# Kernel optimization log

Hardware: AMD Instinct MI355X
Metric: run time of the kernel (lower is better)

The kernel has to match this reference:

```python
import jax, jax.numpy as jnp
import numpy as np


def setup_inputs() -> dict:
    key = jax.random.key(0)
    k1, k2 = jax.random.split(key)
    B, S, D, K = 16, 2048, 256, 512
    features = jax.random.normal(k1, (B, S, D), dtype=jnp.float32)
    Ck = jax.random.normal(k2, (1, K, D), dtype=jnp.float32)
    return {"features": features, "Ck": Ck}


def reference(features, Ck):
    # features: (B, S, D); Ck: (1, K, D)
    # Squared euclidean distance to each of K centers: (B, S, K)
    # Computed as ||f||^2 + ||c||^2 - 2 f.c to avoid the (B*S, K, D) diff tensor.
    C = Ck[0]                                   # (K, D)
    f_sq = jnp.sum(features * features, axis=-1, keepdims=True)   # (B, S, 1)
    c_sq = jnp.sum(C * C, axis=-1)                                # (K,)
    cross = jnp.einsum("bsd,kd->bsk", features, C)               # (B, S, K)
    return f_sq + c_sq[None, None, :] - 2.0 * cross
```

## Files before the change

### kernel.cpp

```cpp
#include <hip/hip_runtime.h>

typedef __attribute__((ext_vector_type(8))) short bf16x8;
typedef __attribute__((ext_vector_type(4))) float f32x4;

#define NCH 8

__device__ inline unsigned short f2bf(float f) {
  unsigned int u = __builtin_bit_cast(unsigned int, f);
  u += 0x7fffu + ((u >> 16) & 1u);
  return (unsigned short)(u >> 16);
}

__device__ inline void gload16(const void* g, void* l) {
  __builtin_amdgcn_global_load_lds(
      (const __attribute__((address_space(1))) void*)g,
      (__attribute__((address_space(3))) void*)l, 16, 0, 0);
}

__global__ void prep_c(const float* __restrict__ C, unsigned short* __restrict__ Cbf,
                       float* __restrict__ csq, int K) {
  const int w = threadIdx.x >> 6, lane = threadIdx.x & 63;
  const int row = blockIdx.x * 4 + w;
  if (row >= K) return;
  const float4 v = *reinterpret_cast<const float4*>(&C[(size_t)row * 256 + lane * 4]);
  ushort4 b;
  b.x = f2bf(v.x); b.y = f2bf(v.y); b.z = f2bf(v.z); b.w = f2bf(v.w);
  const int boff = (lane * 8) ^ ((row & 7) << 4);
  *reinterpret_cast<ushort4*>((char*)Cbf + (size_t)row * 512 + boff) = b;
  float sq = v.x * v.x + v.y * v.y + v.z * v.z + v.w * v.w;
#pragma unroll
  for (int o = 32; o; o >>= 1) sq += __shfl_xor(sq, o);
  if (lane == 0) csq[row] = sq;
}

__global__ __launch_bounds__(256, 2) void dist_fused(
    const float* __restrict__ F, const unsigned short* __restrict__ Cbf,
    const float* __restrict__ csq, float* __restrict__ out, int M, int N) {
  __shared__ __align__(16) char Bs[2][64 * 512];

  const int t = threadIdx.x;
  const int w = t >> 6, l = t & 63;
  const int rl = l & 15, kh = l >> 4;
  const int amask = (rl & 7) << 4;
  const int m0 = blockIdx.x * 64;

  const int srow = t >> 5;
  const int scol = (t & 31) * 16;
  const char* Bsrc = (const char*)Cbf + (size_t)srow * 512 + scol;

#define STAGE(CH, BUF)                                                        \
  {                                                                           \
    _Pragma("unroll")                                                         \
    for (int j = 0; j < 8; ++j)                                               \
      gload16(Bsrc + (size_t)(CH) * 32768 + j * 4096,                         \
              (char*)Bs[BUF] + j * 4096 + t * 16);                            \
  }

  STAGE(0, 0)

  const char* Arow = (const char*)F + (size_t)(m0 + w * 16 + rl) * 1024 + kh * 32;
  f32x4 a0[8], a1[8];
#pragma unroll
  for (int kt = 0; kt < 8; ++kt) {
    a0[kt] = *reinterpret_cast<const f32x4*>(Arow + kt * 128);
    a1[kt] = *reinterpret_cast<const f32x4*>(Arow + kt * 128 + 16);
  }

  bf16x8 af[8];
  float rsq = 0.f;
#pragma unroll
  for (int kt = 0; kt < 8; ++kt) {
    const f32x4 x = a0[kt], y = a1[kt];
    rsq += x[0] * x[0] + x[1] * x[1] + x[2] * x[2] + x[3] * x[3] +
           y[0] * y[0] + y[1] * y[1] + y[2] * y[2] + y[3] * y[3];
    bf16x8 v;
    v[0] = (short)f2bf(x[0]); v[1] = (short)f2bf(x[1]);
    v[2] = (short)f2bf(x[2]); v[3] = (short)f2bf(x[3]);
    v[4] = (short)f2bf(y[0]); v[5] = (short)f2bf(y[1]);
    v[6] = (short)f2bf(y[2]); v[7] = (short)f2bf(y[3]);
    af[kt] = v;
  }
  float fv = rsq;
  fv += __shfl_xor(fv, 16);
  fv += __shfl_xor(fv, 32);

  asm volatile("s_waitcnt vmcnt(0)" ::: "memory");
  __builtin_amdgcn_s_barrier();
  asm volatile("" ::: "memory");

#pragma unroll
  for (int c = 0; c < NCH; ++c) {
    const int cur = c & 1;
    if (c < NCH - 1) {
      STAGE(c + 1, cur ^ 1)
      asm volatile("s_waitcnt vmcnt(8)" ::: "memory");
    } else {
      asm volatile("s_waitcnt vmcnt(0)" ::: "memory");
    }
    __builtin_amdgcn_s_barrier();
    asm volatile("" ::: "memory");

    f32x4 acc[4];
#pragma unroll
    for (int ni = 0; ni < 4; ni++) acc[ni] = (f32x4){0.f, 0.f, 0.f, 0.f};

#pragma unroll
    for (int ni = 0; ni < 4; ni++) {
#pragma unroll
      for (int kt = 0; kt < 8; ++kt) {
        const bf16x8 bfr = *reinterpret_cast<const bf16x8*>(
            (const char*)Bs[cur] + (ni * 16 + rl) * 512 + ((kt * 64 + kh * 16) ^ amask));
        acc[ni] = __builtin_amdgcn_mfma_f32_16x16x32_bf16(bfr, af[kt], acc[ni], 0, 0, 0);
      }
    }

#pragma unroll
    for (int ni = 0; ni < 4; ni++) {
      const int n = c * 64 + ni * 16 + kh * 4;
      const float4 cs4 = *reinterpret_cast<const float4*>(&csq[n]);
      float4 v;
      v.x = fv + cs4.x - 2.0f * acc[ni][0];
      v.y = fv + cs4.y - 2.0f * acc[ni][1];
      v.z = fv + cs4.z - 2.0f * acc[ni][2];
      v.w = fv + cs4.w - 2.0f * acc[ni][3];
      *reinterpret_cast<float4*>(&out[(size_t)(m0 + w * 16 + rl) * N + n]) = v;
    }

    __builtin_amdgcn_s_barrier();
    asm volatile("" ::: "memory");
  }
}

extern "C" void kernel_launch(void* const* d_in, const int* in_sizes, int n_in,
                              void* d_out, int out_size, void* d_ws, size_t ws_size,
                              hipStream_t stream) {
  const float* F = (const float*)d_in[0];
  const float* C = (const float*)d_in[1];
  float* out = (float*)d_out;
  const int D = 256;
  const int M = in_sizes[0] / D;
  const int N = in_sizes[1] / D;

  unsigned short* Cbf = (unsigned short*)d_ws;
  float* csq = (float*)(Cbf + (size_t)N * D);

  hipLaunchKernelGGL(prep_c, dim3(N / 4), dim3(256), 0, stream, C, Cbf, csq, N);
  hipLaunchKernelGGL(dist_fused, dim3(M / 64), dim3(256), 0, stream,
                     F, Cbf, csq, out, M, N);
}
```

Measured before the change: 34.58 us.

## Read centers directly from global and stage output through per-wave LDS

Drops the block-wide double-buffered LDS staging of bf16 centers (and its swizzle in prep_c) and has each wave load B fragments straight from global/L2. The output tile is now staged through a small per-wave LDS buffer, so each row writes 256 contiguous bytes instead of scattered 16-byte pieces. Block barriers go away and the occupancy hint rises to 3 blocks per CU. The trade-off is redundant global loads of the centers by every wave, which now rely on cache hits.

```diff
diff --git a/kernel.cpp b/kernel.cpp
--- a/kernel.cpp
+++ b/kernel.cpp
@@ -3,18 +3,10 @@
 typedef __attribute__((ext_vector_type(8))) short bf16x8;
 typedef __attribute__((ext_vector_type(4))) float f32x4;
 
-#define NCH 8
-
 __device__ inline unsigned short f2bf(float f) {
   unsigned int u = __builtin_bit_cast(unsigned int, f);
   u += 0x7fffu + ((u >> 16) & 1u);
   return (unsigned short)(u >> 16);
-}
-
-__device__ inline void gload16(const void* g, void* l) {
-  __builtin_amdgcn_global_load_lds(
-      (const __attribute__((address_space(1))) void*)g,
-      (__attribute__((address_space(3))) void*)l, 16, 0, 0);
 }
 
 __global__ void prep_c(const float* __restrict__ C, unsigned short* __restrict__ Cbf,
@@ -25,40 +17,25 @@
   const float4 v = *reinterpret_cast<const float4*>(&C[(size_t)row * 256 + lane * 4]);
   ushort4 b;
   b.x = f2bf(v.x); b.y = f2bf(v.y); b.z = f2bf(v.z); b.w = f2bf(v.w);
-  const int boff = (lane * 8) ^ ((row & 7) << 4);
-  *reinterpret_cast<ushort4*>((char*)Cbf + (size_t)row * 512 + boff) = b;
+  *reinterpret_cast<ushort4*>(&Cbf[(size_t)row * 256 + lane * 4]) = b;
   float sq = v.x * v.x + v.y * v.y + v.z * v.z + v.w * v.w;
 #pragma unroll
   for (int o = 32; o; o >>= 1) sq += __shfl_xor(sq, o);
   if (lane == 0) csq[row] = sq;
 }
 
-__global__ __launch_bounds__(256, 2) void dist_fused(
+__global__ __launch_bounds__(256, 3) void dist_fused(
     const float* __restrict__ F, const unsigned short* __restrict__ Cbf,
     const float* __restrict__ csq, float* __restrict__ out, int M, int N) {
-  __shared__ __align__(16) char Bs[2][64 * 512];
+  __shared__ __align__(16) char stg[4][16 * 272];
 
   const int t = threadIdx.x;
   const int w = t >> 6, l = t & 63;
   const int rl = l & 15, kh = l >> 4;
-  const int amask = (rl & 7) << 4;
   const int m0 = blockIdx.x * 64;
+  const int mrow = m0 + w * 16 + rl;
 
-  const int srow = t >> 5;
-  const int scol = (t & 31) * 16;
-  const char* Bsrc = (const char*)Cbf + (size_t)srow * 512 + scol;
-
-#define STAGE(CH, BUF)                                                        \
-  {                                                                           \
-    _Pragma("unroll")                                                         \
-    for (int j = 0; j < 8; ++j)                                               \
-      gload16(Bsrc + (size_t)(CH) * 32768 + j * 4096,                         \
-              (char*)Bs[BUF] + j * 4096 + t * 16);                            \
-  }
-
-  STAGE(0, 0)
-
-  const char* Arow = (const char*)F + (size_t)(m0 + w * 16 + rl) * 1024 + kh * 32;
+  const char* Arow = (const char*)F + (size_t)mrow * 1024 + kh * 32;
   f32x4 a0[8], a1[8];
 #pragma unroll
   for (int kt = 0; kt < 8; ++kt) {
@@ -84,50 +61,43 @@
   fv += __shfl_xor(fv, 16);
   fv += __shfl_xor(fv, 32);
 
-  asm volatile("s_waitcnt vmcnt(0)" ::: "memory");
-  __builtin_amdgcn_s_barrier();
-  asm volatile("" ::: "memory");
+  const char* Bbase = (const char*)Cbf + (size_t)rl * 512 + kh * 16;
+  char* sw = stg[w];
+
+  for (int ng = 0; ng < 8; ++ng) {
+    f32x4 acc[4];
+#pragma unroll
+    for (int nig = 0; nig < 4; ++nig) acc[nig] = (f32x4){0.f, 0.f, 0.f, 0.f};
 
 #pragma unroll
-  for (int c = 0; c < NCH; ++c) {
-    const int cur = c & 1;
-    if (c < NCH - 1) {
-      STAGE(c + 1, cur ^ 1)
-      asm volatile("s_waitcnt vmcnt(8)" ::: "memory");
-    } else {
-      asm volatile("s_waitcnt vmcnt(0)" ::: "memory");
-    }
-    __builtin_amdgcn_s_barrier();
-    asm volatile("" ::: "memory");
-
-    f32x4 acc[4];
-#pragma unroll
-    for (int ni = 0; ni < 4; ni++) acc[ni] = (f32x4){0.f, 0.f, 0.f, 0.f};
-
-#pragma unroll
-    for (int ni = 0; ni < 4; ni++) {
+    for (int nig = 0; nig < 4; ++nig) {
+      const char* bp = Bbase + (size_t)(ng * 4 + nig) * 8192;
 #pragma unroll
       for (int kt = 0; kt < 8; ++kt) {
-        const bf16x8 bfr = *reinterpret_cast<const bf16x8*>(
-            (const char*)Bs[cur] + (ni * 16 + rl) * 512 + ((kt * 64 + kh * 16) ^ amask));
-        acc[ni] = __builtin_amdgcn_mfma_f32_16x16x32_bf16(bfr, af[kt], acc[ni], 0, 0, 0);
+        const bf16x8 bfr = *reinterpret_cast<const bf16x8*>(bp + kt * 64);
+        acc[nig] = __builtin_amdgcn_mfma_f32_16x16x32_bf16(bfr, af[kt], acc[nig], 0, 0, 0);
       }
     }
 
 #pragma unroll
-    for (int ni = 0; ni < 4; ni++) {
-      const int n = c * 64 + ni * 16 + kh * 4;
+    for (int nig = 0; nig < 4; ++nig) {
+      const int n = ng * 64 + nig * 16 + kh * 4;
       const float4 cs4 = *reinterpret_cast<const float4*>(&csq[n]);
       float4 v;
-      v.x = fv + cs4.x - 2.0f * acc[ni][0];
-      v.y = fv + cs4.y - 2.0f * acc[ni][1];
-      v.z = fv + cs4.z - 2.0f * acc[ni][2];
-      v.w = fv + cs4.w - 2.0f * acc[ni][3];
-      *reinterpret_cast<float4*>(&out[(size_t)(m0 + w * 16 + rl) * N + n]) = v;
+      v.x = fv + cs4.x - 2.0f * acc[nig][0];
+      v.y = fv + cs4.y - 2.0f * acc[nig][1];
+      v.z = fv + cs4.z - 2.0f * acc[nig][2];
+      v.w = fv + cs4.w - 2.0f * acc[nig][3];
+      *reinterpret_cast<float4*>(sw + rl * 272 + nig * 64 + kh * 16) = v;
     }
 
-    __builtin_amdgcn_s_barrier();
-    asm volatile("" ::: "memory");
+#pragma unroll
+    for (int p = 0; p < 4; ++p) {
+      const int r16 = p * 4 + kh;
+      const float4 v = *reinterpret_cast<const float4*>(sw + r16 * 272 + rl * 16);
+      *reinterpret_cast<float4*>(
+          &out[(size_t)(m0 + w * 16 + r16) * N + ng * 64 + rl * 4]) = v;
+    }
   }
 }
 
```

After: 78.99 us. 128% more time.

## Split N across two workgroups per row tile with XCD-aware block remap

Applied to the files above, without the earlier changes.

Each workgroup now computes 64 rows by 256 of the 512 centers. This doubles the grid and halves the LDS buffers, so launch bounds can allow four blocks per CU. A block-index remap spreads work across the eight XCDs, and the center norms are staged into LDS. The cost is that every feature tile is loaded and converted to bf16 twice, once by each half-N block, which adds read traffic and conversion work.

```diff
diff --git a/kernel.cpp b/kernel.cpp
--- a/kernel.cpp
+++ b/kernel.cpp
@@ -33,32 +33,39 @@
   if (lane == 0) csq[row] = sq;
 }
 
-__global__ __launch_bounds__(256, 2) void dist_fused(
+__global__ __launch_bounds__(256, 4) void dist_fused(
     const float* __restrict__ F, const unsigned short* __restrict__ Cbf,
     const float* __restrict__ csq, float* __restrict__ out, int M, int N) {
-  __shared__ __align__(16) char Bs[2][64 * 512];
+  __shared__ __align__(16) char Bs[2][32 * 512];
+  __shared__ __align__(16) float csq_s[256];
 
   const int t = threadIdx.x;
   const int w = t >> 6, l = t & 63;
   const int rl = l & 15, kh = l >> 4;
   const int amask = (rl & 7) << 4;
-  const int m0 = blockIdx.x * 64;
+
+  const int workid = (blockIdx.x & 7) * 128 + (blockIdx.x >> 3);
+  const int m0 = (workid >> 1) * 64;
+  const int n0 = (workid & 1) * 256;
+  const int mrow = m0 + w * 16 + rl;
 
   const int srow = t >> 5;
   const int scol = (t & 31) * 16;
-  const char* Bsrc = (const char*)Cbf + (size_t)srow * 512 + scol;
+  const char* Bsrc = (const char*)Cbf + (size_t)(n0 + srow) * 512 + scol;
 
 #define STAGE(CH, BUF)                                                        \
   {                                                                           \
     _Pragma("unroll")                                                         \
-    for (int j = 0; j < 8; ++j)                                               \
-      gload16(Bsrc + (size_t)(CH) * 32768 + j * 4096,                         \
+    for (int j = 0; j < 4; ++j)                                               \
+      gload16(Bsrc + (size_t)(CH) * 16384 + j * 4096,                         \
               (char*)Bs[BUF] + j * 4096 + t * 16);                            \
   }
 
   STAGE(0, 0)
+  if (t < 64)
+    gload16((const char*)csq + (size_t)n0 * 4 + t * 16, (char*)csq_s + t * 16);
 
-  const char* Arow = (const char*)F + (size_t)(m0 + w * 16 + rl) * 1024 + kh * 32;
+  const char* Arow = (const char*)F + (size_t)mrow * 1024 + kh * 32;
   f32x4 a0[8], a1[8];
 #pragma unroll
   for (int kt = 0; kt < 8; ++kt) {
@@ -79,6 +86,7 @@
     v[4] = (short)f2bf(y[0]); v[5] = (short)f2bf(y[1]);
     v[6] = (short)f2bf(y[2]); v[7] = (short)f2bf(y[3]);
     af[kt] = v;
+    asm volatile("" : "+v"(af[kt]));
   }
   float fv = rsq;
   fv += __shfl_xor(fv, 16);
@@ -93,37 +101,31 @@
     const int cur = c & 1;
     if (c < NCH - 1) {
       STAGE(c + 1, cur ^ 1)
-      asm volatile("s_waitcnt vmcnt(8)" ::: "memory");
+      asm volatile("s_waitcnt vmcnt(4)" ::: "memory");
     } else {
       asm volatile("s_waitcnt vmcnt(0)" ::: "memory");
     }
     __builtin_amdgcn_s_barrier();
     asm volatile("" ::: "memory");
 
-    f32x4 acc[4];
 #pragma unroll
-    for (int ni = 0; ni < 4; ni++) acc[ni] = (f32x4){0.f, 0.f, 0.f, 0.f};
-
-#pragma unroll
-    for (int ni = 0; ni < 4; ni++) {
+    for (int ni = 0; ni < 2; ++ni) {
+      f32x4 acc = (f32x4){0.f, 0.f, 0.f, 0.f};
 #pragma unroll
       for (int kt = 0; kt < 8; ++kt) {
         const bf16x8 bfr = *reinterpret_cast<const bf16x8*>(
             (const char*)Bs[cur] + (ni * 16 + rl) * 512 + ((kt * 64 + kh * 16) ^ amask));
-        acc[ni] = __builtin_amdgcn_mfma_f32_16x16x32_bf16(bfr, af[kt], acc[ni], 0, 0, 0);
+        acc = __builtin_amdgcn_mfma_f32_16x16x32_bf16(bfr, af[kt], acc, 0, 0, 0);
       }
-    }
-
-#pragma unroll
-    for (int ni = 0; ni < 4; ni++) {
-      const int n = c * 64 + ni * 16 + kh * 4;
-      const float4 cs4 = *reinterpret_cast<const float4*>(&csq[n]);
+      const int nloc = c * 32 + ni * 16 + kh * 4;
+      const float4 cs4 = *reinterpret_cast<const float4*>(
+          (const char*)csq_s + (size_t)nloc * 4);
       float4 v;
-      v.x = fv + cs4.x - 2.0f * acc[ni][0];
-      v.y = fv + cs4.y - 2.0f * acc[ni][1];
-      v.z = fv + cs4.z - 2.0f * acc[ni][2];
-      v.w = fv + cs4.w - 2.0f * acc[ni][3];
-      *reinterpret_cast<float4*>(&out[(size_t)(m0 + w * 16 + rl) * N + n]) = v;
+      v.x = fv + cs4.x - 2.0f * acc[0];
+      v.y = fv + cs4.y - 2.0f * acc[1];
+      v.z = fv + cs4.z - 2.0f * acc[2];
+      v.w = fv + cs4.w - 2.0f * acc[3];
+      *reinterpret_cast<float4*>(&out[(size_t)mrow * N + n0 + nloc]) = v;
     }
 
     __builtin_amdgcn_s_barrier();
@@ -145,6 +147,7 @@
   float* csq = (float*)(Cbf + (size_t)N * D);
 
   hipLaunchKernelGGL(prep_c, dim3(N / 4), dim3(256), 0, stream, C, Cbf, csq, N);
-  hipLaunchKernelGGL(dist_fused, dim3(M / 64), dim3(256), 0, stream,
+  const int nwg = (M / 64) * 2;
+  hipLaunchKernelGGL(dist_fused, dim3(nwg), dim3(256), 0, stream,
                      F, Cbf, csq, out, M, N);
 }
```

After: 34.05 us. Within noise of the previous version (-1.5%).
